# Kernel optimization log

Measured on AMD Instinct MI355X. Metric: run time of the kernel, lower is better.

The kernel has to match this reference:

```python
import jax, jax.numpy as jnp
import numpy as np

N = 50000
E = 1_600_000
H = 4
IN_F = 256
OUT_F = 32
NEG_SLOPE = 0.2
EPS = 1e-8


def setup_inputs() -> dict:
    key = jax.random.key(0)
    k1, k2, k3, k4, k5 = jax.random.split(key, 5)
    x = jax.random.normal(k1, (N, IN_F), dtype=jnp.float32)
    edge_index = jax.random.randint(k2, (2, E), 0, N, dtype=jnp.int64)
    # Xavier-uniform-like scale for params
    wb = float(np.sqrt(6.0 / (IN_F + OUT_F)))
    ab = float(np.sqrt(6.0 / (OUT_F + 1)))
    W = jax.random.uniform(k3, (H, IN_F, OUT_F), dtype=jnp.float32, minval=-wb, maxval=wb)
    a_l = jax.random.uniform(k4, (H, OUT_F, 1), dtype=jnp.float32, minval=-ab, maxval=ab)
    a_r = jax.random.uniform(k5, (H, OUT_F, 1), dtype=jnp.float32, minval=-ab, maxval=ab)
    return {"x": x, "edge_index": edge_index, "W": W, "a_l": a_l, "a_r": a_r}


def reference(x, edge_index, W, a_l, a_r):
    n = x.shape[0]
    h = jnp.einsum('ni,hio->nho', x, W)                      # (N, H, O)
    attn_l = jnp.einsum('nho,hol->nh', h, a_l)               # (N, H)
    attn_r = jnp.einsum('nho,hol->nh', h, a_r)               # (N, H)
    src, dst = edge_index[0], edge_index[1]
    e = attn_l[src] + attn_r[dst]                            # (E, H)
    e = jnp.where(e >= 0, e, NEG_SLOPE * e)                  # leaky_relu
    # segment softmax over edges grouped by dst (global max, as in source)
    e_exp = jnp.exp(e - jnp.max(e))
    e_sum = jax.ops.segment_sum(e_exp, dst, num_segments=n)  # (N, H)
    alpha = e_exp / (e_sum[dst] + EPS)                       # (E, H)
    msg = h[src] * alpha[:, :, None]                         # (E, H, O)
    out = jax.ops.segment_sum(msg, dst, num_segments=n)      # (N, H, O)
    return out.reshape(n, H * OUT_F)                         # concat=True
```

## Files before the change

kernel.cpp:

```cpp
#include <hip/hip_runtime.h>

#define NN   50000
#define NE   1600000
#define FOUT 128
#define NCH  256
#define EPC  6250
#define NW   12500
#define LOG2E 1.4426950408889634f

typedef short s16x8 __attribute__((ext_vector_type(8)));
typedef float f32x4 __attribute__((ext_vector_type(4)));

#define OFF_M      0u
#define OFF_ROWPTR 16u
#define OFF_ROWCNT 50036u
#define OFF_C8     100036u
#define OFF_SEGB   3300036u
#define OFF_CSR    3400036u
#define OFF_H      4200036u
#define OFF_ATTL   7400036u
#define OFF_ATTR   7600036u
#define OFF_BP     7800036u
#define OFF_BQ     7816420u

__device__ __forceinline__ unsigned short f2bf(float f) {
  unsigned u = __float_as_uint(f);
  u += 0x7FFFu + ((u >> 16) & 1u);
  return (unsigned short)(u >> 16);
}
__device__ __forceinline__ unsigned cvtpk(float lo, float hi) {
  unsigned r;
  asm("v_cvt_pk_bf16_f32 %0, %1, %2" : "=v"(r) : "v"(lo), "v"(hi));
  return r;
}
__device__ __forceinline__ unsigned enc_f32(float f) {
  unsigned u = __float_as_uint(f);
  return (u & 0x80000000u) ? ~u : (u | 0x80000000u);
}
__device__ __forceinline__ float dec_f32(unsigned u) {
  u = (u & 0x80000000u) ? (u & 0x7fffffffu) : ~u;
  return __uint_as_float(u);
}

__global__ __launch_bounds__(256) void k_repack(const float* __restrict__ W,
                                                unsigned* __restrict__ Bp) {
  const int f = blockIdx.x * 256 + threadIdx.x;
  const int s = f >> 9;
  const int c = (f >> 6) & 7;
  const int l = f & 63;
  const int hd = c >> 1;
  const int colw = (c & 1) * 16 + (l & 15);
  const int kb = s * 32 + (l >> 4) * 8;
  unsigned short t[8];
#pragma unroll
  for (int j = 0; j < 8; ++j)
    t[j] = f2bf(W[hd * 8192 + (kb + j) * 32 + colw]);
  uint4 o;
  o.x = (unsigned)t[0] | ((unsigned)t[1] << 16);
  o.y = (unsigned)t[2] | ((unsigned)t[3] << 16);
  o.z = (unsigned)t[4] | ((unsigned)t[5] << 16);
  o.w = (unsigned)t[6] | ((unsigned)t[7] << 16);
  reinterpret_cast<uint4*>(Bp)[f] = o;
}

__global__ __launch_bounds__(256) void k_repack2(const float* __restrict__ W,
                                                 const float* __restrict__ a_l,
                                                 const float* __restrict__ a_r,
                                                 unsigned* __restrict__ Bq) {
  const int f = blockIdx.x * 256 + threadIdx.x;
  const int s = f >> 6;
  const int l = f & 63;
  const int col = l & 15;
  const int kb = s * 32 + (l >> 4) * 8;
  unsigned short t[8];
  if (col < 8) {
    const int hd = col & 3;
    const float* av = (col < 4 ? a_l : a_r) + hd * 32;
#pragma unroll
    for (int j = 0; j < 8; ++j) {
      const float* wr = W + hd * 8192 + (size_t)(kb + j) * 32;
      float dot = 0.f;
#pragma unroll
      for (int o = 0; o < 32; ++o) dot = fmaf(wr[o], av[o], dot);
      t[j] = f2bf(dot * LOG2E);
    }
  } else {
#pragma unroll
    for (int j = 0; j < 8; ++j) t[j] = 0;
  }
  uint4 o;
  o.x = (unsigned)t[0] | ((unsigned)t[1] << 16);
  o.y = (unsigned)t[2] | ((unsigned)t[3] << 16);
  o.z = (unsigned)t[4] | ((unsigned)t[5] << 16);
  o.w = (unsigned)t[6] | ((unsigned)t[7] << 16);
  reinterpret_cast<uint4*>(Bq)[f] = o;
}

__global__ __launch_bounds__(256) void k_gemm(const float* __restrict__ x,
                                              const uint4* __restrict__ Bp,
                                              const uint4* __restrict__ Bq,
                                              unsigned short* __restrict__ h,
                                              float* __restrict__ attl,
                                              float* __restrict__ attr) {
  const int t = threadIdx.x;
  const int wid = t >> 6, l = t & 63;
  const int n0 = (blockIdx.x * 4 + wid) * 16;
  const int lrow = l & 15, g = l >> 4;
  int r0 = n0 + lrow; if (r0 >= NN) r0 = NN - 1;
  const float* x0 = x + (size_t)r0 * 256 + g * 8;
  f32x4 acc[8], acc9;
#pragma unroll
  for (int c = 0; c < 8; ++c) acc[c] = (f32x4){0.f, 0.f, 0.f, 0.f};
  acc9 = (f32x4){0.f, 0.f, 0.f, 0.f};
#pragma unroll
  for (int s = 0; s < 8; ++s) {
    const float4 u0 = *reinterpret_cast<const float4*>(x0 + s * 32);
    const float4 u1 = *reinterpret_cast<const float4*>(x0 + s * 32 + 4);
    union { s16x8 v; unsigned w[4]; } a;
    a.w[0] = cvtpk(u0.x, u0.y);
    a.w[1] = cvtpk(u0.z, u0.w);
    a.w[2] = cvtpk(u1.x, u1.y);
    a.w[3] = cvtpk(u1.z, u1.w);
#pragma unroll
    for (int c = 0; c < 8; ++c) {
      union { uint4 q; s16x8 v; } b;
      b.q = Bp[(s * 8 + c) * 64 + l];
      acc[c] = __builtin_amdgcn_mfma_f32_16x16x32_bf16(a.v, b.v, acc[c], 0, 0, 0);
    }
    union { uint4 q; s16x8 v; } b9;
    b9.q = Bq[s * 64 + l];
    acc9 = __builtin_amdgcn_mfma_f32_16x16x32_bf16(a.v, b9.v, acc9, 0, 0, 0);
  }
#pragma unroll
  for (int c = 0; c < 8; ++c) {
#pragma unroll
    for (int r = 0; r < 4; ++r) {
      const int na = n0 + g * 4 + r;
      if (na < NN) h[(size_t)na * FOUT + c * 16 + lrow] = f2bf(acc[c][r]);
    }
  }
  if (lrow < 8) {
    float* dst = (lrow < 4) ? attl : attr;
    const int hd = lrow & 3;
#pragma unroll
    for (int r = 0; r < 4; ++r) {
      const int na = n0 + g * 4 + r;
      if (na < NN) dst[na * 4 + hd] = acc9[r];
    }
  }
}

__global__ __launch_bounds__(1024) void k_histA(const int* __restrict__ ei,
                                                unsigned* __restrict__ c8) {
  __shared__ unsigned lh[NW];
  const int b = blockIdx.x, t = threadIdx.x;
  for (int w = t; w < NW; w += 1024) lh[w] = 0u;
  __syncthreads();
  const int base = b * EPC;
  for (int k = t; k < EPC; k += 1024) {
    const int d = ei[NE + base + k];
    atomicAdd(&lh[d >> 2], 1u << ((d & 3) * 8));
  }
  __syncthreads();
  for (int w = t; w < NW; w += 1024) c8[(size_t)b * NW + w] = lh[w];
}

__global__ __launch_bounds__(256) void k_cscan1(unsigned* __restrict__ c8,
                                                unsigned* __restrict__ segb) {
  const int b = blockIdx.x;
  const int seg = b / 49;
  const int w = (b % 49) * 256 + threadIdx.x;
  if (w >= NW) return;
  unsigned R = 0;
  const int c0 = seg * 32;
#pragma unroll 4
  for (int c = 0; c < 32; ++c) {
    const unsigned tt = c8[(size_t)(c0 + c) * NW + w];
    c8[(size_t)(c0 + c) * NW + w] = R;
    R += tt;
  }
  segb[seg * NW + w] = R;
}

__global__ __launch_bounds__(256) void k_cscan2(unsigned* __restrict__ segb,
                                                unsigned* __restrict__ rowcnt) {
  const int w = blockIdx.x * 256 + threadIdx.x;
  if (w >= NW) return;
  unsigned R = 0;
#pragma unroll
  for (int s = 0; s < 8; ++s) {
    const unsigned tt = segb[s * NW + w];
    segb[s * NW + w] = R;
    R += tt;
  }
  uint4 rc;
  rc.x = R & 0xffu; rc.y = (R >> 8) & 0xffu; rc.z = (R >> 16) & 0xffu; rc.w = R >> 24;
  reinterpret_cast<uint4*>(rowcnt)[w] = rc;
}

__global__ __launch_bounds__(1024) void k_scan(const unsigned* __restrict__ counts,
                                               unsigned* __restrict__ row_ptr) {
  __shared__ unsigned sums[1024];
  const int t = threadIdx.x;
  const int CH = (NN + 1023) / 1024;
  const int lo = t * CH;
  const int hi = min(lo + CH, NN);
  unsigned s = 0;
#pragma unroll 7
  for (int i = lo; i < hi; ++i) s += counts[i];
  sums[t] = s;
  __syncthreads();
  for (int off = 1; off < 1024; off <<= 1) {
    unsigned v = (t >= off) ? sums[t - off] : 0u;
    __syncthreads();
    sums[t] += v;
    __syncthreads();
  }
  unsigned base = (t == 0) ? 0u : sums[t - 1];
#pragma unroll 7
  for (int i = lo; i < hi; ++i) { row_ptr[i] = base; base += counts[i]; }
  if (t == 0) row_ptr[NN] = sums[1023];
}

__global__ __launch_bounds__(1024) void k_rank(const int* __restrict__ ei,
                                               const unsigned* __restrict__ c8,
                                               const unsigned* __restrict__ segb,
                                               const unsigned* __restrict__ row_ptr,
                                               const float* __restrict__ attl,
                                               const float* __restrict__ attr,
                                               unsigned short* __restrict__ csr,
                                               unsigned* __restrict__ Mslot) {
  __shared__ unsigned lh[NW];
  const int b = blockIdx.x, t = threadIdx.x;
  for (int w = t; w < NW; w += 1024) lh[w] = 0u;
  __syncthreads();
  const int base = b * EPC;
  const unsigned* c8b = c8 + (size_t)b * NW;
  const unsigned* sgb = segb + (size_t)(b >> 5) * NW;
  const float4* AL = reinterpret_cast<const float4*>(attl);
  const float4* AR = reinterpret_cast<const float4*>(attr);
  float m = -3.4e38f;
  for (int k = t; k < EPC; k += 1024) {
    const int e = base + k;
    const int s = ei[e];
    const int d = ei[NE + e];
    const int sh = (d & 3) * 8;
    const unsigned old = atomicAdd(&lh[d >> 2], 1u << sh);
    const unsigned lr = (old >> sh) & 0xffu;
    const unsigned cb = (c8b[d >> 2] >> sh) & 0xffu;
    const unsigned sb = (sgb[d >> 2] >> sh) & 0xffu;
    csr[row_ptr[d] + sb + cb + lr] = (unsigned short)s;
    const float4 a = AL[s];
    const float4 r = AR[d];
    float v0 = a.x + r.x, v1 = a.y + r.y, v2 = a.z + r.z, v3 = a.w + r.w;
    v0 = fmaxf(v0, 0.2f * v0);
    v1 = fmaxf(v1, 0.2f * v1);
    v2 = fmaxf(v2, 0.2f * v2);
    v3 = fmaxf(v3, 0.2f * v3);
    m = fmaxf(m, fmaxf(fmaxf(v0, v1), fmaxf(v2, v3)));
  }
#pragma unroll
  for (int k = 32; k; k >>= 1) m = fmaxf(m, __shfl_xor(m, k));
  if ((t & 63) == 0) atomicMax(Mslot, enc_f32(m));
}

__global__ __launch_bounds__(256) void k_agg(const unsigned short* __restrict__ csr,
                                             const unsigned* __restrict__ row_ptr,
                                             const float* __restrict__ attl,
                                             const float* __restrict__ attr,
                                             const unsigned* __restrict__ hpk,
                                             const unsigned* __restrict__ Mslot,
                                             float* __restrict__ out) {
  const int t = threadIdx.x;
  const int wid = t >> 6, l = t & 63;
  const int q = l & 31;
  const int n = blockIdx.x * 8 + wid * 2 + (l >> 5);
  const int hd = q >> 3;
  const float ar = attr[n * 4 + hd];
  const float epsP = 1e-8f * __builtin_amdgcn_exp2f(dec_f32(*Mslot));
  const unsigned lo = row_ptr[n];
  const int deg = (int)(row_ptr[n + 1] - lo);
  int mdeg = max(deg, __shfl_xor(deg, 32));
  const int nb = (mdeg + 3) >> 2;
  float acc0 = 0.f, acc1 = 0.f, acc2 = 0.f, acc3 = 0.f, wsum = 0.f;

  float alA[4]; uint2 hvA[4];
#define LOADB(BASE, alB, hvB)                                              \
  {                                                                        \
    _Pragma("unroll")                                                      \
    for (int j = 0; j < 4; ++j) {                                          \
      const int i = (BASE) + j;                                            \
      unsigned idx = lo + (unsigned)((i < deg) ? i : 0);                   \
      idx = (idx < NE) ? idx : (NE - 1);                                   \
      const unsigned s = csr[idx];                                         \
      const float a = attl[s * 4 + hd];                                    \
      alB[j] = (i < deg) ? a : -1e30f;                                     \
      hvB[j] = *reinterpret_cast<const uint2*>(&hpk[(size_t)s * 64 + q * 2]); \
    }                                                                      \
  }
#define COMPUTE(alB, hvB)                                                  \
  {                                                                        \
    _Pragma("unroll")                                                      \
    for (int j = 0; j < 4; ++j) {                                          \
      const float v = alB[j] + ar;                                         \
      const float w = __builtin_amdgcn_exp2f(fmaxf(v, 0.2f * v));          \
      wsum += w;                                                           \
      acc0 = fmaf(w, __uint_as_float(hvB[j].x << 16), acc0);               \
      acc1 = fmaf(w, __uint_as_float(hvB[j].x & 0xffff0000u), acc1);       \
      acc2 = fmaf(w, __uint_as_float(hvB[j].y << 16), acc2);               \
      acc3 = fmaf(w, __uint_as_float(hvB[j].y & 0xffff0000u), acc3);       \
    }                                                                      \
  }
  if (nb > 0) {
    LOADB(0, alA, hvA);
    for (int b = 1; b < nb; ++b) {
      float alB[4]; uint2 hvB[4];
      LOADB(b * 4, alB, hvB);
      COMPUTE(alA, hvA);
#pragma unroll
      for (int j = 0; j < 4; ++j) { alA[j] = alB[j]; hvA[j] = hvB[j]; }
    }
    COMPUTE(alA, hvA);
  }
  const float inv = 1.f / (wsum + epsP);
  float4 o;
  o.x = acc0 * inv; o.y = acc1 * inv; o.z = acc2 * inv; o.w = acc3 * inv;
  *reinterpret_cast<float4*>(&out[(size_t)n * FOUT + q * 4]) = o;
#undef LOADB
#undef COMPUTE
}

extern "C" void kernel_launch(void* const* d_in, const int* in_sizes, int n_in,
                              void* d_out, int out_size, void* d_ws, size_t ws_size,
                              hipStream_t stream) {
  const float* x   = (const float*)d_in[0];
  const int*   ei  = (const int*)d_in[1];
  const float* W   = (const float*)d_in[2];
  const float* a_l = (const float*)d_in[3];
  const float* a_r = (const float*)d_in[4];
  float* out = (float*)d_out;
  unsigned* ws = (unsigned*)d_ws;

  unsigned* Mslot   = ws + OFF_M;
  unsigned* row_ptr = ws + OFF_ROWPTR;
  unsigned* rowcnt  = ws + OFF_ROWCNT;
  unsigned* c8      = ws + OFF_C8;
  unsigned* segb    = ws + OFF_SEGB;
  unsigned short* csr = (unsigned short*)(ws + OFF_CSR);
  unsigned short* h = (unsigned short*)(ws + OFF_H);
  float*    attl    = (float*)(ws + OFF_ATTL);
  float*    attr    = (float*)(ws + OFF_ATTR);
  unsigned* Bp      = ws + OFF_BP;
  unsigned* Bq      = ws + OFF_BQ;

  hipMemsetAsync(Mslot, 0, 16 * sizeof(unsigned), stream);

  k_repack <<<16, 256, 0, stream>>>(W, Bp);
  k_repack2<<<2, 256, 0, stream>>>(W, a_l, a_r, Bq);
  k_gemm   <<<(NN + 63) / 64, 256, 0, stream>>>(x, (const uint4*)Bp, (const uint4*)Bq,
                                                h, attl, attr);
  k_histA  <<<NCH, 1024, 0, stream>>>(ei, c8);
  k_cscan1 <<<392, 256, 0, stream>>>(c8, segb);
  k_cscan2 <<<49, 256, 0, stream>>>(segb, rowcnt);
  k_scan   <<<1, 1024, 0, stream>>>(rowcnt, row_ptr);
  k_rank   <<<NCH, 1024, 0, stream>>>(ei, c8, segb, row_ptr, attl, attr, csr, Mslot);
  k_agg    <<<NN / 8, 256, 0, stream>>>(csr, row_ptr, attl, attr,
                                        (const unsigned*)h, Mslot, out);
}
```

Before: 353.0 us.

## Use fixed-stride padded CSR, drop row scan, move max into aggregation with fixup

Replaces the prefix-summed CSR with a fixed-stride slot layout (96 entries per node), which removes the single-block row-pointer scan and the row_ptr lookups. Histogram and rank kernels now split destination nodes into 4 ranges so each block uses a smaller shared histogram and runs at 512 threads. The global max is computed inside the aggregation kernel instead of the rank kernel, so aggregation writes unnormalized sums and a new fixup kernel applies the epsilon-adjusted normalization. This trades an extra pass over the output and redundant edge-list reads for less serialization; it also assumes in-degree never exceeds 96, and the 8-bit degree packing already caps it at 255.

```diff
diff --git a/kernel.cpp b/kernel.cpp
--- a/kernel.cpp
+++ b/kernel.cpp
@@ -1,27 +1,30 @@
 #include <hip/hip_runtime.h>
 
-#define NN   50000
-#define NE   1600000
-#define FOUT 128
-#define NCH  256
-#define EPC  6250
-#define NW   12500
+#define NN    50000
+#define NE    1600000
+#define FOUT  128
+#define NCH   128
+#define EPC   12500
+#define NW    12500
+#define NSPLIT 4
+#define NRNG  12500
+#define NWH   3125
+#define CSTR  96
 #define LOG2E 1.4426950408889634f
 
 typedef short s16x8 __attribute__((ext_vector_type(8)));
 typedef float f32x4 __attribute__((ext_vector_type(4)));
 
 #define OFF_M      0u
-#define OFF_ROWPTR 16u
-#define OFF_ROWCNT 50036u
-#define OFF_C8     100036u
-#define OFF_SEGB   3300036u
-#define OFF_CSR    3400036u
-#define OFF_H      4200036u
-#define OFF_ATTL   7400036u
-#define OFF_ATTR   7600036u
-#define OFF_BP     7800036u
-#define OFF_BQ     7816420u
+#define OFF_DEGP   16u
+#define OFF_SEGB   12516u
+#define OFF_C8     112516u
+#define OFF_CSR    1712516u
+#define OFF_H      4112516u
+#define OFF_ATTL   7312516u
+#define OFF_ATTR   7512516u
+#define OFF_BP     7712516u
+#define OFF_BQ     7728900u
 
 __device__ __forceinline__ unsigned short f2bf(float f) {
   unsigned u = __float_as_uint(f);
@@ -150,19 +153,22 @@
   }
 }
 
-__global__ __launch_bounds__(1024) void k_histA(const int* __restrict__ ei,
-                                                unsigned* __restrict__ c8) {
-  __shared__ unsigned lh[NW];
+__global__ __launch_bounds__(512) void k_histA(const int* __restrict__ ei,
+                                               unsigned* __restrict__ c8) {
+  __shared__ unsigned lh[NWH];
   const int b = blockIdx.x, t = threadIdx.x;
-  for (int w = t; w < NW; w += 1024) lh[w] = 0u;
+  const int chunk = b >> 2, half = b & 3;
+  const unsigned nlo = half * NRNG;
+  for (int w = t; w < NWH; w += 512) lh[w] = 0u;
   __syncthreads();
-  const int base = b * EPC;
-  for (int k = t; k < EPC; k += 1024) {
-    const int d = ei[NE + base + k];
-    atomicAdd(&lh[d >> 2], 1u << ((d & 3) * 8));
+  const int base = chunk * EPC;
+  for (int k = t; k < EPC; k += 512) {
+    const unsigned dl = (unsigned)ei[NE + base + k] - nlo;
+    if (dl < (unsigned)NRNG) atomicAdd(&lh[dl >> 2], 1u << ((dl & 3) * 8));
   }
   __syncthreads();
-  for (int w = t; w < NW; w += 1024) c8[(size_t)b * NW + w] = lh[w];
+  unsigned* dst = c8 + (size_t)chunk * NW + half * NWH;
+  for (int w = t; w < NWH; w += 512) dst[w] = lh[w];
 }
 
 __global__ __launch_bounds__(256) void k_cscan1(unsigned* __restrict__ c8,
@@ -172,9 +178,9 @@
   const int w = (b % 49) * 256 + threadIdx.x;
   if (w >= NW) return;
   unsigned R = 0;
-  const int c0 = seg * 32;
-#pragma unroll 4
-  for (int c = 0; c < 32; ++c) {
+  const int c0 = seg * 16;
+#pragma unroll
+  for (int c = 0; c < 16; ++c) {
     const unsigned tt = c8[(size_t)(c0 + c) * NW + w];
     c8[(size_t)(c0 + c) * NW + w] = R;
     R += tt;
@@ -183,7 +189,7 @@
 }
 
 __global__ __launch_bounds__(256) void k_cscan2(unsigned* __restrict__ segb,
-                                                unsigned* __restrict__ rowcnt) {
+                                                unsigned* __restrict__ degp) {
   const int w = blockIdx.x * 256 + threadIdx.x;
   if (w >= NW) return;
   unsigned R = 0;
@@ -193,96 +199,55 @@
     segb[s * NW + w] = R;
     R += tt;
   }
-  uint4 rc;
-  rc.x = R & 0xffu; rc.y = (R >> 8) & 0xffu; rc.z = (R >> 16) & 0xffu; rc.w = R >> 24;
-  reinterpret_cast<uint4*>(rowcnt)[w] = rc;
-}
-
-__global__ __launch_bounds__(1024) void k_scan(const unsigned* __restrict__ counts,
-                                               unsigned* __restrict__ row_ptr) {
-  __shared__ unsigned sums[1024];
-  const int t = threadIdx.x;
-  const int CH = (NN + 1023) / 1024;
-  const int lo = t * CH;
-  const int hi = min(lo + CH, NN);
-  unsigned s = 0;
-#pragma unroll 7
-  for (int i = lo; i < hi; ++i) s += counts[i];
-  sums[t] = s;
+  degp[w] = R;
+}
+
+__global__ __launch_bounds__(512) void k_rank(const int* __restrict__ ei,
+                                              const unsigned* __restrict__ c8,
+                                              const unsigned* __restrict__ segb,
+                                              unsigned short* __restrict__ csr) {
+  __shared__ unsigned lh[NWH];
+  const int b = blockIdx.x, t = threadIdx.x;
+  const int chunk = b >> 2, half = b & 3;
+  const unsigned nlo = half * NRNG;
+  const unsigned* c8b = c8 + (size_t)chunk * NW + half * NWH;
+  const unsigned* sgb = segb + (size_t)(chunk >> 4) * NW + half * NWH;
+  for (int w = t; w < NWH; w += 512) lh[w] = c8b[w] + sgb[w];
   __syncthreads();
-  for (int off = 1; off < 1024; off <<= 1) {
-    unsigned v = (t >= off) ? sums[t - off] : 0u;
-    __syncthreads();
-    sums[t] += v;
-    __syncthreads();
-  }
-  unsigned base = (t == 0) ? 0u : sums[t - 1];
-#pragma unroll 7
-  for (int i = lo; i < hi; ++i) { row_ptr[i] = base; base += counts[i]; }
-  if (t == 0) row_ptr[NN] = sums[1023];
-}
-
-__global__ __launch_bounds__(1024) void k_rank(const int* __restrict__ ei,
-                                               const unsigned* __restrict__ c8,
-                                               const unsigned* __restrict__ segb,
-                                               const unsigned* __restrict__ row_ptr,
-                                               const float* __restrict__ attl,
-                                               const float* __restrict__ attr,
-                                               unsigned short* __restrict__ csr,
-                                               unsigned* __restrict__ Mslot) {
-  __shared__ unsigned lh[NW];
-  const int b = blockIdx.x, t = threadIdx.x;
-  for (int w = t; w < NW; w += 1024) lh[w] = 0u;
-  __syncthreads();
-  const int base = b * EPC;
-  const unsigned* c8b = c8 + (size_t)b * NW;
-  const unsigned* sgb = segb + (size_t)(b >> 5) * NW;
-  const float4* AL = reinterpret_cast<const float4*>(attl);
-  const float4* AR = reinterpret_cast<const float4*>(attr);
-  float m = -3.4e38f;
-  for (int k = t; k < EPC; k += 1024) {
-    const int e = base + k;
-    const int s = ei[e];
-    const int d = ei[NE + e];
-    const int sh = (d & 3) * 8;
-    const unsigned old = atomicAdd(&lh[d >> 2], 1u << sh);
-    const unsigned lr = (old >> sh) & 0xffu;
-    const unsigned cb = (c8b[d >> 2] >> sh) & 0xffu;
-    const unsigned sb = (sgb[d >> 2] >> sh) & 0xffu;
-    csr[row_ptr[d] + sb + cb + lr] = (unsigned short)s;
-    const float4 a = AL[s];
-    const float4 r = AR[d];
-    float v0 = a.x + r.x, v1 = a.y + r.y, v2 = a.z + r.z, v3 = a.w + r.w;
-    v0 = fmaxf(v0, 0.2f * v0);
-    v1 = fmaxf(v1, 0.2f * v1);
-    v2 = fmaxf(v2, 0.2f * v2);
-    v3 = fmaxf(v3, 0.2f * v3);
-    m = fmaxf(m, fmaxf(fmaxf(v0, v1), fmaxf(v2, v3)));
-  }
-#pragma unroll
-  for (int k = 32; k; k >>= 1) m = fmaxf(m, __shfl_xor(m, k));
-  if ((t & 63) == 0) atomicMax(Mslot, enc_f32(m));
+  const int base = chunk * EPC;
+  for (int k = t; k < EPC; k += 512) {
+    const int d = ei[NE + base + k];
+    const unsigned dl = (unsigned)d - nlo;
+    if (dl < (unsigned)NRNG) {
+      const int s = ei[base + k];
+      const int sh = (dl & 3) * 8;
+      const unsigned old = atomicAdd(&lh[dl >> 2], 1u << sh);
+      csr[(size_t)d * CSTR + ((old >> sh) & 0xffu)] = (unsigned short)s;
+    }
+  }
 }
 
 __global__ __launch_bounds__(256) void k_agg(const unsigned short* __restrict__ csr,
-                                             const unsigned* __restrict__ row_ptr,
+                                             const unsigned* __restrict__ degp,
                                              const float* __restrict__ attl,
                                              const float* __restrict__ attr,
                                              const unsigned* __restrict__ hpk,
-                                             const unsigned* __restrict__ Mslot,
-                                             float* __restrict__ out) {
+                                             float* __restrict__ outac,
+                                             float* __restrict__ wsbuf,
+                                             unsigned* __restrict__ Mslot) {
+  __shared__ float wmax[4];
   const int t = threadIdx.x;
   const int wid = t >> 6, l = t & 63;
   const int q = l & 31;
   const int n = blockIdx.x * 8 + wid * 2 + (l >> 5);
   const int hd = q >> 3;
   const float ar = attr[n * 4 + hd];
-  const float epsP = 1e-8f * __builtin_amdgcn_exp2f(dec_f32(*Mslot));
-  const unsigned lo = row_ptr[n];
-  const int deg = (int)(row_ptr[n + 1] - lo);
+  const int deg = (int)((degp[n >> 2] >> ((n & 3) * 8)) & 0xffu);
+  const unsigned lo = (unsigned)n * CSTR;
   int mdeg = max(deg, __shfl_xor(deg, 32));
   const int nb = (mdeg + 3) >> 2;
   float acc0 = 0.f, acc1 = 0.f, acc2 = 0.f, acc3 = 0.f, wsum = 0.f;
+  float mlk = -3.4e38f;
 
   float alA[4]; uint2 hvA[4];
 #define LOADB(BASE, alB, hvB)                                              \
@@ -290,8 +255,7 @@
     _Pragma("unroll")                                                      \
     for (int j = 0; j < 4; ++j) {                                          \
       const int i = (BASE) + j;                                            \
-      unsigned idx = lo + (unsigned)((i < deg) ? i : 0);                   \
-      idx = (idx < NE) ? idx : (NE - 1);                                   \
+      const unsigned idx = lo + (unsigned)((i < deg) ? i : 0);             \
       const unsigned s = csr[idx];                                         \
       const float a = attl[s * 4 + hd];                                    \
       alB[j] = (i < deg) ? a : -1e30f;                                     \
@@ -303,7 +267,9 @@
     _Pragma("unroll")                                                      \
     for (int j = 0; j < 4; ++j) {                                          \
       const float v = alB[j] + ar;                                         \
-      const float w = __builtin_amdgcn_exp2f(fmaxf(v, 0.2f * v));          \
+      const float lk = fmaxf(v, 0.2f * v);                                 \
+      mlk = fmaxf(mlk, lk);                                                \
+      const float w = __builtin_amdgcn_exp2f(lk);                          \
       wsum += w;                                                           \
       acc0 = fmaf(w, __uint_as_float(hvB[j].x << 16), acc0);               \
       acc1 = fmaf(w, __uint_as_float(hvB[j].x & 0xffff0000u), acc1);       \
@@ -322,12 +288,33 @@
     }
     COMPUTE(alA, hvA);
   }
-  const float inv = 1.f / (wsum + epsP);
   float4 o;
-  o.x = acc0 * inv; o.y = acc1 * inv; o.z = acc2 * inv; o.w = acc3 * inv;
-  *reinterpret_cast<float4*>(&out[(size_t)n * FOUT + q * 4]) = o;
+  o.x = acc0; o.y = acc1; o.z = acc2; o.w = acc3;
+  *reinterpret_cast<float4*>(&outac[(size_t)n * FOUT + q * 4]) = o;
+  if ((q & 7) == 0) wsbuf[n * 4 + hd] = wsum;
+#pragma unroll
+  for (int m = 1; m < 64; m <<= 1) mlk = fmaxf(mlk, __shfl_xor(mlk, m));
+  if (l == 0) wmax[wid] = mlk;
+  __syncthreads();
+  if (t == 0) {
+    const float m = fmaxf(fmaxf(wmax[0], wmax[1]), fmaxf(wmax[2], wmax[3]));
+    atomicMax(Mslot, enc_f32(m));
+  }
 #undef LOADB
 #undef COMPUTE
+}
+
+__global__ __launch_bounds__(256) void k_fix(const float* __restrict__ wsbuf,
+                                             const unsigned* __restrict__ Mslot,
+                                             float4* __restrict__ outv) {
+  const int f = blockIdx.x * 256 + threadIdx.x;
+  const int n = f >> 5, c = f & 31, hd = c >> 3;
+  const float eps2 = 1e-8f * __builtin_amdgcn_exp2f(dec_f32(*Mslot));
+  const float w = wsbuf[n * 4 + hd];
+  const float inv = 1.f / (w + eps2);
+  float4 a = outv[f];
+  a.x *= inv; a.y *= inv; a.z *= inv; a.w *= inv;
+  outv[f] = a;
 }
 
 extern "C" void kernel_launch(void* const* d_in, const int* in_sizes, int n_in,
@@ -342,10 +329,10 @@
   unsigned* ws = (unsigned*)d_ws;
 
   unsigned* Mslot   = ws + OFF_M;
-  unsigned* row_ptr = ws + OFF_ROWPTR;
-  unsigned* rowcnt  = ws + OFF_ROWCNT;
+  unsigned* degp    = ws + OFF_DEGP;
+  unsigned* segb    = ws + OFF_SEGB;
   unsigned* c8      = ws + OFF_C8;
-  unsigned* segb    = ws + OFF_SEGB;
+  float*    wsbuf   = (float*)(ws + OFF_C8);
   unsigned short* csr = (unsigned short*)(ws + OFF_CSR);
   unsigned short* h = (unsigned short*)(ws + OFF_H);
   float*    attl    = (float*)(ws + OFF_ATTL);
@@ -359,11 +346,11 @@
   k_repack2<<<2, 256, 0, stream>>>(W, a_l, a_r, Bq);
   k_gemm   <<<(NN + 63) / 64, 256, 0, stream>>>(x, (const uint4*)Bp, (const uint4*)Bq,
                                                 h, attl, attr);
-  k_histA  <<<NCH, 1024, 0, stream>>>(ei, c8);
+  k_histA  <<<NCH * NSPLIT, 512, 0, stream>>>(ei, c8);
   k_cscan1 <<<392, 256, 0, stream>>>(c8, segb);
-  k_cscan2 <<<49, 256, 0, stream>>>(segb, rowcnt);
-  k_scan   <<<1, 1024, 0, stream>>>(rowcnt, row_ptr);
-  k_rank   <<<NCH, 1024, 0, stream>>>(ei, c8, segb, row_ptr, attl, attr, csr, Mslot);
-  k_agg    <<<NN / 8, 256, 0, stream>>>(csr, row_ptr, attl, attr,
-                                        (const unsigned*)h, Mslot, out);
-}
+  k_cscan2 <<<49, 256, 0, stream>>>(segb, degp);
+  k_rank   <<<NCH * NSPLIT, 512, 0, stream>>>(ei, c8, segb, csr);
+  k_agg    <<<NN / 8, 256, 0, stream>>>(csr, degp, attl, attr,
+                                        (const unsigned*)h, out, wsbuf, Mslot);
+  k_fix    <<<6250, 256, 0, stream>>>(wsbuf, Mslot, (float4*)out);
+}
```

Result: faster. 310.5 us (-12.1%).
